# Optimization experiments

Hardware: AMD Instinct MI355X
Metric: run time of the kernel (lower is better)

Reference implementation:

```python
import jax, jax.numpy as jnp
import numpy as np

B, S, H = 2, 2048, 1024
NH, NKV, HD = 16, 4, 64
Q_SIZE = NH * HD          # 1024
KV_SIZE = NKV * HD        # 256
R_SOFTPLUS_0 = 1.442695041
NEG = -2.3819763e38  # large negative for masking (matches float32 -inf-ish additive mask)


def setup_inputs() -> dict:
    key = jax.random.key(0)
    k1, k2, k3, k4, k5, k6 = jax.random.split(key, 6)
    hidden_states = jax.random.normal(k1, (B, S, H), dtype=jnp.float32)
    # causal additive mask [B, 1, S, S]
    causal = jnp.tril(jnp.ones((S, S), dtype=bool))
    mask = jnp.where(causal, 0.0, NEG).astype(jnp.float32)
    mask = jnp.broadcast_to(mask[None, None], (B, 1, S, S))
    fan = 1.0 / np.sqrt(H)
    qkv_w = jax.random.uniform(k2, ((NH + 2 * NKV) * HD, H), jnp.float32, -fan, fan)
    qkv_b = jax.random.uniform(k3, ((NH + 2 * NKV) * HD,), jnp.float32, -fan, fan)
    fo = 1.0 / np.sqrt(Q_SIZE)
    o_w = jax.random.uniform(k4, (H, Q_SIZE), jnp.float32, -fo, fo)
    o_b = jax.random.uniform(k5, (H,), jnp.float32, -fo, fo)
    scaling = jax.random.normal(k6, (HD,), dtype=jnp.float32)
    return {"hidden_states": hidden_states, "mask": mask, "scaling": scaling,
            "qkv_w": qkv_w, "qkv_b": qkv_b, "o_w": o_w, "o_b": o_b}


def reference(hidden_states, mask, scaling, qkv_w, qkv_b, o_w, o_b):
    b, s, _ = hidden_states.shape
    q_w, k_w, v_w = qkv_w[:Q_SIZE], qkv_w[Q_SIZE:Q_SIZE + KV_SIZE], qkv_w[-KV_SIZE:]
    q_b, k_b, v_b = qkv_b[:Q_SIZE], qkv_b[Q_SIZE:Q_SIZE + KV_SIZE], qkv_b[-KV_SIZE:]
    xq = (hidden_states @ q_w.T + q_b).reshape(b, s, NH, HD)
    # per-dim softplus scaling fused into q
    scale = (R_SOFTPLUS_0 / np.sqrt(HD)) * jax.nn.softplus(scaling)
    xq = xq * scale[None, None, None, :]
    xk = (hidden_states @ k_w.T + k_b).reshape(b, s, NKV, HD)
    xv = (hidden_states @ v_w.T + v_b).reshape(b, s, NKV, HD)
    # GQA: repeat kv heads (repeat_interleave along head dim)
    key = jnp.repeat(xk, NH // NKV, axis=2)   # [b, s, NH, HD]
    value = jnp.repeat(xv, NH // NKV, axis=2)
    scores = jnp.einsum('bqhd,bkhd->bhqk', xq, key) + mask
    scores = jax.nn.softmax(scores.astype(jnp.float32), axis=-1).astype(xq.dtype)
    out = jnp.einsum('bhqk,bkhd->bqhd', scores, value).reshape(b, s, NH * HD)
    out = out @ o_w.T + o_b
    return scores, out
```

## Files before the change

### kernel.cpp

```cpp
#include <hip/hip_runtime.h>
#include <hip/hip_bf16.h>
#include <cstdint>
#include <cstddef>

typedef __attribute__((ext_vector_type(4))) float f32x4;
typedef __attribute__((ext_vector_type(8))) short bf16x8;

#define DEVI static __device__ __forceinline__

DEVI unsigned short f2bf(float f) {
  union { float f; unsigned int u; } v; v.f = f;
  unsigned int u = v.u;
  unsigned int r = (u + 0x7fffu + ((u >> 16) & 1u)) >> 16;
  return (unsigned short)r;
}

DEVI unsigned int cvt_pk(float lo, float hi) {
  unsigned int r;
  asm("v_cvt_pk_bf16_f32 %0, %1, %2" : "=v"(r) : "v"(lo), "v"(hi));
  return r;
}

DEVI f32x4 mfma16(bf16x8 a, bf16x8 b, f32x4 c) {
  return __builtin_amdgcn_mfma_f32_16x16x32_bf16(a, b, c, 0, 0, 0);
}

#define GLDS(gp, lp) __builtin_amdgcn_global_load_lds(                         \
    (const __attribute__((address_space(1))) void*)(const void*)(gp),          \
    (__attribute__((address_space(3))) void*)(void*)(lp), 16, 0, 0)

#define SBAR() asm volatile("s_barrier" ::: "memory")
#define WV(n) asm volatile("s_waitcnt vmcnt(" #n ")" ::: "memory")
#define FORCE4(x) asm volatile("" : "+v"(x))

__global__ void convert_kernel(const float* __restrict__ hidden,
                               const float* __restrict__ qkv_w,
                               const float* __restrict__ o_w,
                               const float* __restrict__ scaling,
                               unsigned short* __restrict__ hbf,
                               unsigned short* __restrict__ wbf,
                               unsigned short* __restrict__ obf,
                               float* __restrict__ qscale) {
  int tid = blockIdx.x * blockDim.x + threadIdx.x;
  int nt = gridDim.x * blockDim.x;
  if (tid < 64) {
    float x = scaling[tid];
    float sp = (x > 20.f) ? x : log1pf(__expf(x));
    qscale[tid] = 0.1803368801243369f * 1.4426950408889634f * sp;
  }
  for (int i = tid; i < 1048576; i += nt) {
    float4 v = ((const float4*)hidden)[i];
    ushort4 o = { f2bf(v.x), f2bf(v.y), f2bf(v.z), f2bf(v.w) };
    ((ushort4*)hbf)[i] = o;
  }
  for (int i = tid; i < 393216; i += nt) {
    float4 v = ((const float4*)qkv_w)[i];
    ushort4 o = { f2bf(v.x), f2bf(v.y), f2bf(v.z), f2bf(v.w) };
    ((ushort4*)wbf)[i] = o;
  }
  for (int i = tid; i < 262144; i += nt) {
    float4 v = ((const float4*)o_w)[i];
    ushort4 o = { f2bf(v.x), f2bf(v.y), f2bf(v.z), f2bf(v.w) };
    ((ushort4*)obf)[i] = o;
  }
}

__global__ __launch_bounds__(256, 2) void gemm_kernel(
    const unsigned short* __restrict__ A,
    const unsigned short* __restrict__ Bw,
    const float* __restrict__ bias,
    const float* __restrict__ qscale,
    unsigned short* __restrict__ oq,
    unsigned short* __restrict__ okv,
    unsigned short* __restrict__ ovt) {
  __shared__ __align__(16) unsigned short sA[128 * 64];
  __shared__ __align__(16) unsigned short sB[128 * 64];
  const int t = threadIdx.x, lane = t & 63, w = t >> 6;
  const int l15 = lane & 15, lg = lane >> 4;
  const int m0 = blockIdx.y * 128, n0 = blockIdx.x * 128;
  const int wr = w >> 1, wc = w & 1;

  f32x4 acc[4][4] = {};

  for (int kb = 0; kb < 1024; kb += 64) {
    __syncthreads();
#pragma unroll
    for (int i = 0; i < 4; i++) {
      int idx = i * 256 + w * 64 + lane;
      int row = idx >> 3;
      int cg = (idx & 7) ^ (row & 7);
      GLDS(A + (size_t)(m0 + row) * 1024 + kb + cg * 8, sA + (i * 256 + w * 64) * 8);
      GLDS(Bw + (size_t)(n0 + row) * 1024 + kb + cg * 8, sB + (i * 256 + w * 64) * 8);
    }
    __syncthreads();
    bf16x8 af[4][2], bfr[4][2];
#pragma unroll
    for (int rt = 0; rt < 4; rt++) {
      int row = wr * 64 + rt * 16 + l15;
#pragma unroll
      for (int kk = 0; kk < 2; kk++) {
        int c = (kk * 4 + lg) ^ (row & 7);
        af[rt][kk] = *(const bf16x8*)((const char*)sA + row * 128 + c * 16);
      }
      int rowb = wc * 64 + rt * 16 + l15;
#pragma unroll
      for (int kk = 0; kk < 2; kk++) {
        int c = (kk * 4 + lg) ^ (rowb & 7);
        bfr[rt][kk] = *(const bf16x8*)((const char*)sB + rowb * 128 + c * 16);
      }
    }
#pragma unroll
    for (int kk = 0; kk < 2; kk++)
#pragma unroll
      for (int rt = 0; rt < 4; rt++)
#pragma unroll
        for (int ct = 0; ct < 4; ct++)
          acc[rt][ct] = mfma16(af[rt][kk], bfr[ct][kk], acc[rt][ct]);
  }

#pragma unroll
  for (int rt = 0; rt < 4; rt++) {
#pragma unroll
    for (int ct = 0; ct < 4; ct++) {
      int n = n0 + wc * 64 + ct * 16 + l15;
      float bv = bias[n];
#pragma unroll
      for (int jj = 0; jj < 4; jj++) {
        int m = m0 + wr * 64 + rt * 16 + lg * 4 + jj;
        float v = acc[rt][ct][jj] + bv;
        int b = m >> 11, s = m & 2047;
        if (n < 1024) {
          int h = n >> 6, d = n & 63;
          v *= qscale[d];
          oq[(((size_t)(b * 16 + h) * 2048 + s) << 6) + d] = f2bf(v);
        } else if (n < 1280) {
          int kv = (n - 1024) >> 6, d = n & 63;
          okv[(((size_t)(b * 4 + kv) * 2048 + s) << 6) + d] = f2bf(v);
        } else {
          int kv = (n - 1280) >> 6, d = n & 63;
          ovt[(((size_t)((b * 4 + kv) * 64 + d)) << 11) + s] = f2bf(v);
        }
      }
    }
  }
}

__global__ __launch_bounds__(256, 2) void gemm2_kernel(
    const unsigned short* __restrict__ A,
    const unsigned short* __restrict__ Bw,
    const float* __restrict__ bias,
    float* __restrict__ of) {
  __shared__ __align__(16) unsigned short sA[64 * 64];
  __shared__ __align__(16) unsigned short sB[128 * 64];
  const int t = threadIdx.x, lane = t & 63, w = t >> 6;
  const int l15 = lane & 15, lg = lane >> 4;
  const int m0 = blockIdx.y * 64, n0 = blockIdx.x * 128;
  const int wr = w >> 1, wc = w & 1;

  f32x4 acc[2][4] = {};

  for (int kb = 0; kb < 1024; kb += 64) {
    __syncthreads();
#pragma unroll
    for (int i = 0; i < 2; i++) {
      int idx = i * 256 + w * 64 + lane;
      int row = idx >> 3;
      int cg = (idx & 7) ^ (row & 7);
      GLDS(A + (size_t)(m0 + row) * 1024 + kb + cg * 8, sA + (i * 256 + w * 64) * 8);
    }
#pragma unroll
    for (int i = 0; i < 4; i++) {
      int idx = i * 256 + w * 64 + lane;
      int row = idx >> 3;
      int cg = (idx & 7) ^ (row & 7);
      GLDS(Bw + (size_t)(n0 + row) * 1024 + kb + cg * 8, sB + (i * 256 + w * 64) * 8);
    }
    __syncthreads();
    bf16x8 af[2][2], bfr[4][2];
#pragma unroll
    for (int rt = 0; rt < 2; rt++) {
      int row = wr * 32 + rt * 16 + l15;
#pragma unroll
      for (int kk = 0; kk < 2; kk++) {
        int c = (kk * 4 + lg) ^ (row & 7);
        af[rt][kk] = *(const bf16x8*)((const char*)sA + row * 128 + c * 16);
      }
    }
#pragma unroll
    for (int ct = 0; ct < 4; ct++) {
      int rowb = wc * 64 + ct * 16 + l15;
#pragma unroll
      for (int kk = 0; kk < 2; kk++) {
        int c = (kk * 4 + lg) ^ (rowb & 7);
        bfr[ct][kk] = *(const bf16x8*)((const char*)sB + rowb * 128 + c * 16);
      }
    }
#pragma unroll
    for (int kk = 0; kk < 2; kk++)
#pragma unroll
      for (int rt = 0; rt < 2; rt++)
#pragma unroll
        for (int ct = 0; ct < 4; ct++)
          acc[rt][ct] = mfma16(af[rt][kk], bfr[ct][kk], acc[rt][ct]);
  }

#pragma unroll
  for (int rt = 0; rt < 2; rt++) {
#pragma unroll
    for (int ct = 0; ct < 4; ct++) {
      int n = n0 + wc * 64 + ct * 16 + l15;
      float bv = bias[n];
#pragma unroll
      for (int jj = 0; jj < 4; jj++) {
        int m = m0 + wr * 32 + rt * 16 + lg * 4 + jj;
        of[(size_t)m * 1024 + n] = acc[rt][ct][jj] + bv;
      }
    }
  }
}

__global__ __launch_bounds__(256, 2) void attn_kernel(
    const unsigned short* __restrict__ q_ws,
    const unsigned short* __restrict__ k_ws,
    const unsigned short* __restrict__ v_ws,
    float* __restrict__ scores,
    unsigned short* __restrict__ attn_bf) {
  __shared__ __align__(16) unsigned short sK[4][4096];
  __shared__ __align__(16) unsigned short sVT[4][4096];
  __shared__ __align__(16) unsigned char sP[4][2048];

  const int t = threadIdx.x, lane = t & 63, w = t >> 6;
  const int l15 = lane & 15, lg = lane >> 4;
  int bid = blockIdx.x;
  int bh = bid & 31;
  int pr = bid >> 5;
  int p = (bid < 256) ? pr : (23 - pr);
  int b = bh >> 4, h = bh & 15, kv = h >> 2;
  const int qtA = p, qtB = 31 - p;
  const int NB = qtB + 1;
  const int start = bid & 15;

  const unsigned short* Kp = k_ws + ((size_t)(b * 4 + kv) * 2048) * 64;
  const unsigned short* Vp = v_ws + ((size_t)(b * 4 + kv) * 64) * 2048;
  const int qrA = qtA * 64 + w * 16 + l15;
  const int qrB = qtB * 64 + w * 16 + l15;

  auto rot = [&](int j) { int n = j + start; return (n >= NB) ? n - NB : n; };

  bf16x8 aqA[2], aqB[2];
  {
    const unsigned short* qa = q_ws + ((size_t)bh * 2048 + qrA) * 64;
    const unsigned short* qb = q_ws + ((size_t)bh * 2048 + qrB) * 64;
    aqA[0] = *(const bf16x8*)(qa + lg * 8);
    aqA[1] = *(const bf16x8*)(qa + 32 + lg * 8);
    aqB[0] = *(const bf16x8*)(qb + lg * 8);
    aqB[1] = *(const bf16x8*)(qb + 32 + lg * 8);
    FORCE4(*(f32x4*)&aqA[0]); FORCE4(*(f32x4*)&aqA[1]);
    FORCE4(*(f32x4*)&aqB[0]); FORCE4(*(f32x4*)&aqB[1]);
  }

  auto stageK = [&](int kt, int bufi) {
#pragma unroll
    for (int i = 0; i < 2; i++) {
      int idx = i * 256 + w * 64 + lane;
      int row = idx >> 3;
      int cg = (idx & 7) ^ (row & 7);
      GLDS(Kp + (size_t)(kt * 64 + row) * 64 + cg * 8, sK[bufi] + (i * 256 + w * 64) * 8);
    }
  };
  auto stageVT = [&](int kt, int bufi) {
#pragma unroll
    for (int i = 0; i < 2; i++) {
      int idx = i * 256 + w * 64 + lane;
      int row = idx >> 3;
      int cg = (idx & 7) ^ (row & 7);
      GLDS(Vp + (size_t)row * 2048 + kt * 64 + cg * 8, sVT[bufi] + (i * 256 + w * 64) * 8);
    }
  };
  auto qk_tile = [&](const unsigned short* kb, const bf16x8(&aq)[2], f32x4(&acc)[4]) {
#pragma unroll
    for (int ct = 0; ct < 4; ct++) {
      int row = ct * 16 + l15;
#pragma unroll
      for (int kk = 0; kk < 2; kk++) {
        int c = (kk * 4 + lg) ^ (row & 7);
        bf16x8 ak = *(const bf16x8*)((const char*)kb + row * 128 + c * 16);
        acc[ct] = mfma16(ak, aq[kk], acc[ct]);
      }
    }
  };

  stageK(rot(0), 0);
  stageK(rot(1), 1);
  float rsA = 0.f, rsB = 0.f;
  for (int j = 0; j < NB; j++) {
    const int n = rot(j);
    if (j + 2 < NB) { stageK(rot(j + 2), (j + 2) & 3); WV(4); }
    else if (j + 1 < NB) { WV(2); }
    else { WV(0); }
    SBAR();
    const unsigned short* kb = sK[j & 3];
    {
      f32x4 acc[4] = {};
      qk_tile(kb, aqB, acc);
      if (n < NB - 1) {
#pragma unroll
        for (int ct = 0; ct < 4; ct++)
#pragma unroll
          for (int jj = 0; jj < 4; jj++) rsB += __builtin_amdgcn_exp2f(acc[ct][jj]);
      } else {
#pragma unroll
        for (int ct = 0; ct < 4; ct++) {
          int kb0 = n * 64 + ct * 16 + lg * 4;
#pragma unroll
          for (int jj = 0; jj < 4; jj++)
            rsB += (kb0 + jj <= qrB) ? __builtin_amdgcn_exp2f(acc[ct][jj]) : 0.f;
        }
      }
    }
    if (n <= qtA) {
      f32x4 acc[4] = {};
      qk_tile(kb, aqA, acc);
      if (n < qtA) {
#pragma unroll
        for (int ct = 0; ct < 4; ct++)
#pragma unroll
          for (int jj = 0; jj < 4; jj++) rsA += __builtin_amdgcn_exp2f(acc[ct][jj]);
      } else {
#pragma unroll
        for (int ct = 0; ct < 4; ct++) {
          int kb0 = n * 64 + ct * 16 + lg * 4;
#pragma unroll
          for (int jj = 0; jj < 4; jj++)
            rsA += (kb0 + jj <= qrA) ? __builtin_amdgcn_exp2f(acc[ct][jj]) : 0.f;
        }
      }
    }
  }
  rsA += __shfl_xor(rsA, 16); rsA += __shfl_xor(rsA, 32);
  rsB += __shfl_xor(rsB, 16); rsB += __shfl_xor(rsB, 32);
  float rinvA = 1.0f / rsA, rinvB = 1.0f / rsB;

  SBAR();

  stageK(rot(0), 0); stageVT(rot(0), 0);
  stageK(rot(1), 1); stageVT(rot(1), 1);
  f32x4 accoA[4] = {}, accoB[4] = {};
  unsigned char* myP = &sP[w][0];
  const int xr = (l15 & 7) << 4;
  float* SpA = scores + ((size_t)bh * 2048 + qtA * 64) * 2048;
  float* SpB = scores + ((size_t)bh * 2048 + qtB * 64) * 2048;

  for (int j = 0; j < NB; j++) {
    const int n = rot(j);
    if (j + 2 < NB) { stageK(rot(j + 2), (j + 2) & 3); stageVT(rot(j + 2), (j + 2) & 3); }
    if (j == 0) { WV(8); }
    else if (j == 1) { WV(16); }
    else if (j + 2 < NB) { WV(24); }
    else if (j + 1 < NB) { WV(20); }
    else { WV(16); }
    SBAR();
    const unsigned short* kb = sK[j & 3];
    const unsigned short* vt = sVT[j & 3];
    int k0 = n * 64;

    {
      f32x4 acc[4] = {};
      qk_tile(kb, aqB, acc);
      if (n == NB - 1) {
#pragma unroll
        for (int ct = 0; ct < 4; ct++) {
          int kb0 = k0 + ct * 16 + lg * 4;
#pragma unroll
          for (int jj = 0; jj < 4; jj++)
            acc[ct][jj] = (kb0 + jj <= qrB) ? __builtin_amdgcn_exp2f(acc[ct][jj]) * rinvB : 0.f;
        }
      } else {
#pragma unroll
        for (int ct = 0; ct < 4; ct++)
#pragma unroll
          for (int jj = 0; jj < 4; jj++)
            acc[ct][jj] = __builtin_amdgcn_exp2f(acc[ct][jj]) * rinvB;
      }
      float* srow = SpB + (size_t)(w * 16 + l15) * 2048 + k0 + lg * 4;
#pragma unroll
      for (int ct = 0; ct < 4; ct++) *(f32x4*)(srow + ct * 16) = acc[ct];
#pragma unroll
      for (int ct = 0; ct < 4; ct++) {
        uint2 pw;
        pw.x = cvt_pk(acc[ct][0], acc[ct][1]);
        pw.y = cvt_pk(acc[ct][2], acc[ct][3]);
        *(uint2*)(myP + l15 * 128 + ((ct * 32 + lg * 8) ^ xr)) = pw;
      }
#pragma unroll
      for (int kk = 0; kk < 2; kk++) {
        bf16x8 ap = *(const bf16x8*)(myP + l15 * 128 + ((kk * 64 + lg * 16) ^ xr));
#pragma unroll
        for (int ct = 0; ct < 4; ct++) {
          int vrow = ct * 16 + l15;
          int cv = (kk * 4 + lg) ^ (vrow & 7);
          bf16x8 bv = *(const bf16x8*)((const char*)vt + vrow * 128 + cv * 16);
          accoB[ct] = mfma16(bv, ap, accoB[ct]);
        }
      }
    }

    if (n <= qtA) {
      f32x4 acc[4] = {};
      qk_tile(kb, aqA, acc);
      if (n == qtA) {
#pragma unroll
        for (int ct = 0; ct < 4; ct++) {
          int kb0 = k0 + ct * 16 + lg * 4;
#pragma unroll
          for (int jj = 0; jj < 4; jj++)
            acc[ct][jj] = (kb0 + jj <= qrA) ? __builtin_amdgcn_exp2f(acc[ct][jj]) * rinvA : 0.f;
        }
      } else {
#pragma unroll
        for (int ct = 0; ct < 4; ct++)
#pragma unroll
          for (int jj = 0; jj < 4; jj++)
            acc[ct][jj] = __builtin_amdgcn_exp2f(acc[ct][jj]) * rinvA;
      }
      float* srow = SpA + (size_t)(w * 16 + l15) * 2048 + k0 + lg * 4;
#pragma unroll
      for (int ct = 0; ct < 4; ct++) *(f32x4*)(srow + ct * 16) = acc[ct];
#pragma unroll
      for (int ct = 0; ct < 4; ct++) {
        uint2 pw;
        pw.x = cvt_pk(acc[ct][0], acc[ct][1]);
        pw.y = cvt_pk(acc[ct][2], acc[ct][3]);
        *(uint2*)(myP + l15 * 128 + ((ct * 32 + lg * 8) ^ xr)) = pw;
      }
#pragma unroll
      for (int kk = 0; kk < 2; kk++) {
        bf16x8 ap = *(const bf16x8*)(myP + l15 * 128 + ((kk * 64 + lg * 16) ^ xr));
#pragma unroll
        for (int ct = 0; ct < 4; ct++) {
          int vrow = ct * 16 + l15;
          int cv = (kk * 4 + lg) ^ (vrow & 7);
          bf16x8 bv = *(const bf16x8*)((const char*)vt + vrow * 128 + cv * 16);
          accoA[ct] = mfma16(bv, ap, accoA[ct]);
        }
      }
    } else {
      f32x4 z = {0.f, 0.f, 0.f, 0.f};
      float* srow = SpA + (size_t)(w * 16 + l15) * 2048 + k0 + lg * 4;
#pragma unroll
      for (int ct = 0; ct < 4; ct++) *(f32x4*)(srow + ct * 16) = z;
    }
  }

  {
    int mA = b * 2048 + qtA * 64 + w * 16 + l15;
    int mB = b * 2048 + qtB * 64 + w * 16 + l15;
    unsigned int* oA = (unsigned int*)(attn_bf + (size_t)mA * 1024 + h * 64);
    unsigned int* oB = (unsigned int*)(attn_bf + (size_t)mB * 1024 + h * 64);
#pragma unroll
    for (int ct = 0; ct < 4; ct++) {
      uint2 pa, pb;
      pa.x = cvt_pk(accoA[ct][0], accoA[ct][1]);
      pa.y = cvt_pk(accoA[ct][2], accoA[ct][3]);
      pb.x = cvt_pk(accoB[ct][0], accoB[ct][1]);
      pb.y = cvt_pk(accoB[ct][2], accoB[ct][3]);
      *(uint2*)(oA + (ct * 16 + lg * 4) / 2) = pa;
      *(uint2*)(oB + (ct * 16 + lg * 4) / 2) = pb;
    }
  }

  int zbase = NB * 64;
  if (zbase < 2048) {
    f32x4 z = {0.f, 0.f, 0.f, 0.f};
    float* ra = scores + ((size_t)bh * 2048 + qrA) * 2048;
    float* rb = scores + ((size_t)bh * 2048 + qrB) * 2048;
    for (int c = zbase + lg * 4; c < 2048; c += 16) {
      *(f32x4*)(ra + c) = z;
      *(f32x4*)(rb + c) = z;
    }
  }
}

extern "C" void kernel_launch(void* const* d_in, const int* in_sizes, int n_in,
                              void* d_out, int out_size, void* d_ws, size_t ws_size,
                              hipStream_t stream) {
  const float* hidden  = (const float*)d_in[0];
  const float* scaling = (const float*)d_in[2];
  const float* qkv_w   = (const float*)d_in[3];
  const float* qkv_b   = (const float*)d_in[4];
  const float* o_w     = (const float*)d_in[5];
  const float* o_b     = (const float*)d_in[6];

  float* scores = (float*)d_out;
  float* outp   = (float*)d_out + (size_t)2 * 16 * 2048 * 2048;

  char* ws = (char*)d_ws;
  unsigned short* hidden_bf = (unsigned short*)(ws + 0);
  unsigned short* qkvw_bf   = (unsigned short*)(ws + 8388608);
  unsigned short* ow_bf     = (unsigned short*)(ws + 11534336);
  unsigned short* q_ws      = (unsigned short*)(ws + 13631488);
  unsigned short* k_ws      = (unsigned short*)(ws + 22020096);
  unsigned short* v_ws      = (unsigned short*)(ws + 24117248);
  unsigned short* attn_bf   = (unsigned short*)(ws + 26214400);
  float* qscale             = (float*)(ws + 34603008);

  convert_kernel<<<512, 256, 0, stream>>>(hidden, qkv_w, o_w, scaling,
                                          hidden_bf, qkvw_bf, ow_bf, qscale);
  gemm_kernel<<<dim3(12, 32), 256, 0, stream>>>(hidden_bf, qkvw_bf, qkv_b,
                                                qscale, q_ws, k_ws, v_ws);
  attn_kernel<<<512, 256, 0, stream>>>(q_ws, k_ws, v_ws, scores, attn_bf);
  gemm2_kernel<<<dim3(8, 64), 256, 0, stream>>>(attn_bf, ow_bf, o_b, outp);
}
```

Measured before the change: 200.8 us.

## Transpose score tiles through LDS for coalesced stores; shrink pass-2 to double buffering

Score tiles are now staged through a per-wave LDS scratch area and read back transposed, so each row of the probability output is written with contiguous 16-byte stores across lanes rather than strided per-lane row writes. To make room, the shared memory is unified into one byte array and the second pass drops from four-deep to double-buffered K/V staging with adjusted wait counts, plus a barrier at the end of each iteration. This trades shallower prefetch and an extra block-wide sync per tile for better-coalesced writes of the large scores tensor.

```diff
diff --git a/kernel.cpp b/kernel.cpp
--- a/kernel.cpp
+++ b/kernel.cpp
@@ -225,9 +225,7 @@
     const unsigned short* __restrict__ v_ws,
     float* __restrict__ scores,
     unsigned short* __restrict__ attn_bf) {
-  __shared__ __align__(16) unsigned short sK[4][4096];
-  __shared__ __align__(16) unsigned short sVT[4][4096];
-  __shared__ __align__(16) unsigned char sP[4][2048];
+  __shared__ __align__(16) unsigned char smem[57344];
 
   const int t = threadIdx.x, lane = t & 63, w = t >> 6;
   const int l15 = lane & 15, lg = lane >> 4;
@@ -246,6 +244,10 @@
   const int qrB = qtB * 64 + w * 16 + l15;
 
   auto rot = [&](int j) { int n = j + start; return (n >= NB) ? n - NB : n; };
+  auto kbuf = [&](int i) { return (unsigned short*)(smem + i * 8192); };
+  auto vbuf = [&](int i) { return (unsigned short*)(smem + 32768 + i * 8192); };
+  float* Sw = (float*)(smem + 16384 + w * 4096);
+  unsigned char* myP = smem + 49152 + w * 2048;
 
   bf16x8 aqA[2], aqB[2];
   {
@@ -265,7 +267,7 @@
       int idx = i * 256 + w * 64 + lane;
       int row = idx >> 3;
       int cg = (idx & 7) ^ (row & 7);
-      GLDS(Kp + (size_t)(kt * 64 + row) * 64 + cg * 8, sK[bufi] + (i * 256 + w * 64) * 8);
+      GLDS(Kp + (size_t)(kt * 64 + row) * 64 + cg * 8, kbuf(bufi) + (i * 256 + w * 64) * 8);
     }
   };
   auto stageVT = [&](int kt, int bufi) {
@@ -274,7 +276,7 @@
       int idx = i * 256 + w * 64 + lane;
       int row = idx >> 3;
       int cg = (idx & 7) ^ (row & 7);
-      GLDS(Vp + (size_t)row * 2048 + kt * 64 + cg * 8, sVT[bufi] + (i * 256 + w * 64) * 8);
+      GLDS(Vp + (size_t)row * 2048 + kt * 64 + cg * 8, vbuf(bufi) + (i * 256 + w * 64) * 8);
     }
   };
   auto qk_tile = [&](const unsigned short* kb, const bf16x8(&aq)[2], f32x4(&acc)[4]) {
@@ -287,6 +289,20 @@
         bf16x8 ak = *(const bf16x8*)((const char*)kb + row * 128 + c * 16);
         acc[ct] = mfma16(ak, aq[kk], acc[ct]);
       }
+    }
+  };
+  auto tstore = [&](float* Sp, const f32x4(&acc)[4], int k0) {
+#pragma unroll
+    for (int ct = 0; ct < 4; ct++) {
+      int xs = (ct * 4 + lg) ^ l15;
+      *(f32x4*)(Sw + l15 * 64 + xs * 4) = acc[ct];
+    }
+#pragma unroll
+    for (int i = 0; i < 4; i++) {
+      int r = i * 4 + lg;
+      int xs = l15 ^ r;
+      f32x4 v = *(const f32x4*)(Sw + r * 64 + xs * 4);
+      *(f32x4*)(Sp + (size_t)(w * 16 + r) * 2048 + k0 + l15 * 4) = v;
     }
   };
 
@@ -299,7 +315,7 @@
     else if (j + 1 < NB) { WV(2); }
     else { WV(0); }
     SBAR();
-    const unsigned short* kb = sK[j & 3];
+    const unsigned short* kb = kbuf(j & 3);
     {
       f32x4 acc[4] = {};
       qk_tile(kb, aqB, acc);
@@ -344,24 +360,20 @@
   SBAR();
 
   stageK(rot(0), 0); stageVT(rot(0), 0);
-  stageK(rot(1), 1); stageVT(rot(1), 1);
   f32x4 accoA[4] = {}, accoB[4] = {};
-  unsigned char* myP = &sP[w][0];
   const int xr = (l15 & 7) << 4;
   float* SpA = scores + ((size_t)bh * 2048 + qtA * 64) * 2048;
   float* SpB = scores + ((size_t)bh * 2048 + qtB * 64) * 2048;
 
   for (int j = 0; j < NB; j++) {
     const int n = rot(j);
-    if (j + 2 < NB) { stageK(rot(j + 2), (j + 2) & 3); stageVT(rot(j + 2), (j + 2) & 3); }
-    if (j == 0) { WV(8); }
-    else if (j == 1) { WV(16); }
-    else if (j + 2 < NB) { WV(24); }
-    else if (j + 1 < NB) { WV(20); }
-    else { WV(16); }
+    if (j + 1 < NB) { stageK(rot(j + 1), (j + 1) & 1); stageVT(rot(j + 1), (j + 1) & 1); }
+    if (j == 0) { WV(4); }
+    else if (j + 1 < NB) { WV(12); }
+    else { WV(8); }
     SBAR();
-    const unsigned short* kb = sK[j & 3];
-    const unsigned short* vt = sVT[j & 3];
+    const unsigned short* kb = kbuf(j & 1);
+    const unsigned short* vt = vbuf(j & 1);
     int k0 = n * 64;
 
     {
@@ -382,9 +394,7 @@
           for (int jj = 0; jj < 4; jj++)
             acc[ct][jj] = __builtin_amdgcn_exp2f(acc[ct][jj]) * rinvB;
       }
-      float* srow = SpB + (size_t)(w * 16 + l15) * 2048 + k0 + lg * 4;
-#pragma unroll
-      for (int ct = 0; ct < 4; ct++) *(f32x4*)(srow + ct * 16) = acc[ct];
+      tstore(SpB, acc, k0);
 #pragma unroll
       for (int ct = 0; ct < 4; ct++) {
         uint2 pw;
@@ -423,9 +433,7 @@
           for (int jj = 0; jj < 4; jj++)
             acc[ct][jj] = __builtin_amdgcn_exp2f(acc[ct][jj]) * rinvA;
       }
-      float* srow = SpA + (size_t)(w * 16 + l15) * 2048 + k0 + lg * 4;
-#pragma unroll
-      for (int ct = 0; ct < 4; ct++) *(f32x4*)(srow + ct * 16) = acc[ct];
+      tstore(SpA, acc, k0);
 #pragma unroll
       for (int ct = 0; ct < 4; ct++) {
         uint2 pw;
@@ -446,10 +454,13 @@
       }
     } else {
       f32x4 z = {0.f, 0.f, 0.f, 0.f};
-      float* srow = SpA + (size_t)(w * 16 + l15) * 2048 + k0 + lg * 4;
-#pragma unroll
-      for (int ct = 0; ct < 4; ct++) *(f32x4*)(srow + ct * 16) = z;
-    }
+#pragma unroll
+      for (int i = 0; i < 4; i++) {
+        int r = i * 4 + lg;
+        *(f32x4*)(SpA + (size_t)(w * 16 + r) * 2048 + k0 + l15 * 4) = z;
+      }
+    }
+    SBAR();
   }
 
   {
```

Result: faster. 194.6 us (-3.1%).
